# Optimization experiments

Hardware: AMD Instinct MI355X
Metric: run time of the kernel (lower is better)

Reference implementation:

```python
import jax, jax.numpy as jnp
import numpy as np

N_NODES = 100000
N_EDGES = 1600000
N_GRAPHS = 256
DIMS = [128, 128, 128, 128]  # gcn_layers_dim -> 3 GCNConv layers


def setup_inputs() -> dict:
    key = jax.random.key(0)
    ks = jax.random.split(key, 12)
    inp = {
        "x": jax.random.normal(ks[0], (N_NODES, DIMS[0]), jnp.float32),
        "edge_index": jax.random.randint(ks[1], (2, N_EDGES), 0, N_NODES),
        "edge_weight": jax.random.uniform(ks[2], (N_EDGES,), jnp.float32),
        "batch": jnp.sort(jax.random.randint(ks[3], (N_NODES,), 0, N_GRAPHS)),
    }
    for i in range(3):
        fan_in = DIMS[i]
        scale = 1.0 / np.sqrt(fan_in)
        inp[f"W{i+1}"] = jax.random.uniform(ks[4 + 2 * i], (DIMS[i], DIMS[i + 1]),
                                             jnp.float32, -scale, scale)
        inp[f"b{i+1}"] = jax.random.uniform(ks[5 + 2 * i], (DIMS[i + 1],),
                                             jnp.float32, -scale, scale)
    return inp


def reference(x, edge_index, edge_weight, batch, W1, b1, W2, b2, W3, b3):
    n = x.shape[0]
    # PyG GCNConv: add self-loops with weight 1, symmetric normalization.
    loop = jnp.arange(n)
    row = jnp.concatenate([edge_index[0], loop])  # source nodes
    col = jnp.concatenate([edge_index[1], loop])  # target nodes (aggregation index)
    w = jnp.concatenate([edge_weight, jnp.ones((n,), x.dtype)])
    deg = jax.ops.segment_sum(w, col, num_segments=n)
    dinv = jnp.where(deg > 0, jax.lax.rsqrt(deg), jnp.zeros_like(deg))
    norm = dinv[row] * w * dinv[col]  # [E+N]

    # global_mean_pool setup
    counts = jax.ops.segment_sum(jnp.ones((n,), x.dtype), batch,
                                 num_segments=N_GRAPHS)
    counts = jnp.maximum(counts, 1.0)[:, None]

    def gcn_conv(h, W, b):
        hl = h @ W                      # linear projection first (PyG order)
        msg = hl[row] * norm[:, None]   # gather + edge scaling
        out = jax.ops.segment_sum(msg, col, num_segments=n)  # scatter-add
        return out + b

    embeddings = []
    h = x
    for W, b in ((W1, b1), (W2, b2), (W3, b3)):
        h = gcn_conv(h, W, b)
        h = jax.nn.relu(h)              # relu_layers_index = [0,1,2]
        emb = jax.ops.segment_sum(h, batch, num_segments=N_GRAPHS) / counts
        embeddings.append(emb)          # gep = global_mean_pool
    return tuple(embeddings)
```

## Files before the change

### kernel.cpp

```cpp
#include <hip/hip_runtime.h>


typedef short short8 __attribute__((ext_vector_type(8)));
typedef float f32x4  __attribute__((ext_vector_type(4)));

__device__ inline unsigned pack_bf16x2(float a, float b) {
    unsigned ua = __float_as_uint(a);
    ua = (ua + 0x7FFFu + ((ua >> 16) & 1u)) >> 16;
    unsigned ub = __float_as_uint(b);
    ub = (ub + 0x7FFFu + ((ub >> 16) & 1u)) >> 16;
    return ua | (ub << 16);
}
__device__ inline ushort bf16_1(float a) {
    unsigned ua = __float_as_uint(a);
    return (ushort)((ua + 0x7FFFu + ((ua >> 16) & 1u)) >> 16);
}
__device__ inline float bf_lo(unsigned u) { return __uint_as_float(u << 16); }
__device__ inline float bf_hi(unsigned u) { return __uint_as_float(u & 0xFFFF0000u); }


template <bool F32IN>
__device__ __forceinline__ void gemm_tile(const void* __restrict__ Hin,
                                          const ushort* __restrict__ WbT,
                                          unsigned* __restrict__ O, int M,
                                          int bid, unsigned* sOut) {
    int lane = threadIdx.x & 63;
    int wv = threadIdx.x >> 6;
    int quad = lane >> 4;
    int mrow = lane & 15;
    int m0 = bid * 128 + wv * 32;
    int r0 = m0 + mrow;
    int r1 = r0 + 16;
    int r0c = r0 < M ? r0 : M - 1;
    int r1c = r1 < M ? r1 : M - 1;

    short8 a0[4], a1[4];
    if (F32IN) {
        const float* Hf = (const float*)Hin;
#pragma unroll
        for (int s = 0; s < 4; s++) {
            const float4* p0 = (const float4*)(Hf + (size_t)r0c * 128 + s * 32 + quad * 8);
            const float4* p1 = (const float4*)(Hf + (size_t)r1c * 128 + s * 32 + quad * 8);
            float4 f0 = p0[0], f1 = p0[1];
            float4 g0 = p1[0], g1 = p1[1];
            union { short8 s8; unsigned u[4]; } t0, t1;
            t0.u[0] = pack_bf16x2(f0.x, f0.y); t0.u[1] = pack_bf16x2(f0.z, f0.w);
            t0.u[2] = pack_bf16x2(f1.x, f1.y); t0.u[3] = pack_bf16x2(f1.z, f1.w);
            t1.u[0] = pack_bf16x2(g0.x, g0.y); t1.u[1] = pack_bf16x2(g0.z, g0.w);
            t1.u[2] = pack_bf16x2(g1.x, g1.y); t1.u[3] = pack_bf16x2(g1.z, g1.w);
            a0[s] = t0.s8; a1[s] = t1.s8;
        }
    } else {
        const unsigned* Hb = (const unsigned*)Hin;
#pragma unroll
        for (int s = 0; s < 4; s++) {
            a0[s] = *(const short8*)(Hb + (size_t)r0c * 64 + s * 16 + quad * 4);
            a1[s] = *(const short8*)(Hb + (size_t)r1c * 64 + s * 16 + quad * 4);
        }
    }
    f32x4 acc0[8], acc1[8];
#pragma unroll
    for (int t = 0; t < 8; t++) {
        acc0[t] = (f32x4){0.f, 0.f, 0.f, 0.f};
        acc1[t] = (f32x4){0.f, 0.f, 0.f, 0.f};
    }
#pragma unroll
    for (int s = 0; s < 4; s++) {
#pragma unroll
        for (int t = 0; t < 8; t++) {
            short8 b = *(const short8*)(WbT + (t * 16 + mrow) * 128 + s * 32 + quad * 8);
            acc0[t] = __builtin_amdgcn_mfma_f32_16x16x32_bf16(a0[s], b, acc0[t], 0, 0, 0);
            acc1[t] = __builtin_amdgcn_mfma_f32_16x16x32_bf16(a1[s], b, acc1[t], 0, 0, 0);
        }
    }
    ushort* so = (ushort*)(sOut + wv * 32 * 64);
#pragma unroll
    for (int t = 0; t < 8; t++) {
#pragma unroll
        for (int r = 0; r < 4; r++) {
            int lr = quad * 4 + r;
            int c = t * 16 + mrow;
            so[lr * 128 + c] = bf16_1(acc0[t][r]);
            so[(lr + 16) * 128 + c] = bf16_1(acc1[t][r]);
        }
    }
    __syncthreads();
    const unsigned* si = sOut + wv * 32 * 64;
#pragma unroll 8
    for (int r = 0; r < 32; r++) {
        int row = m0 + r;
        if (row < M) O[(size_t)row * 64 + lane] = si[r * 64 + lane];
    }
}

__device__ __forceinline__ void pool_tile(const unsigned* __restrict__ HB,
                                          const int* __restrict__ gb,
                                          float* __restrict__ outp, int g,
                                          float* part) {
    int lane = threadIdx.x & 63, w = threadIdx.x >> 6;
    int s = gb[g], e = gb[g + 1];
    float ax = 0.f, ay = 0.f;
    for (int i = s + w; i < e; i += 4) {
        unsigned u = HB[(size_t)i * 64 + lane];
        ax += bf_lo(u); ay += bf_hi(u);
    }
    part[w * 128 + lane * 2] = ax;
    part[w * 128 + lane * 2 + 1] = ay;
    __syncthreads();
    if (threadIdx.x < 128) {
        float sum = part[threadIdx.x] + part[128 + threadIdx.x]
                  + part[256 + threadIdx.x] + part[384 + threadIdx.x];
        float c = (float)(e - s);
        outp[g * 128 + threadIdx.x] = sum / fmaxf(c, 1.0f);
    }
}


__global__ void k_prep(const int* __restrict__ batch, int* __restrict__ gb,
                       int G, int N,
                       const float* __restrict__ W0, const float* __restrict__ W1,
                       const float* __restrict__ W2, ushort* __restrict__ WbT) {
    int id = blockIdx.x * blockDim.x + threadIdx.x;
    if (id <= G) {
        int lo = 0, hi = N;
        while (lo < hi) { int mid = (lo + hi) >> 1; if (batch[mid] < id) lo = mid + 1; else hi = mid; }
        gb[id] = lo;
    }
    if (id < 3 * 16384) {
        int l = id >> 14;
        const float* W = (l == 0) ? W0 : ((l == 1) ? W1 : W2);
        int id2 = id & 16383;
        int n = id2 & 127, k = id2 >> 7;
        WbT[l * 16384 + n * 128 + k] = bf16_1(W[k * 128 + n]);
    }
}

__global__ __launch_bounds__(256) void k_phase1(const int* __restrict__ ei,
                                                int* __restrict__ hist, int E,
                                                const float* __restrict__ x,
                                                const ushort* __restrict__ WbT,
                                                unsigned* __restrict__ O, int M,
                                                int nbGemm, int nbCount) {
    __shared__ unsigned sBuf[8192];
    if (blockIdx.x < nbGemm) {
        gemm_tile<true>(x, WbT, O, M, blockIdx.x, sBuf);
        return;
    }
    int blk = blockIdx.x - nbGemm;
    unsigned* hcnt = sBuf;
    int t = threadIdx.x;
    for (int i = t; i < nbGemm; i += 256) hcnt[i] = 0;
    __syncthreads();
    int base = blk * 8192;
    for (int i = t; i < 8192; i += 256) {
        int e = base + i;
        if (e < E) atomicAdd(&hcnt[(unsigned)ei[E + e] >> 7], 1u);
    }
    __syncthreads();
    for (int b = t; b < nbGemm; b += 256)
        hist[b * nbCount + blk] = (int)hcnt[b];
}

__global__ __launch_bounds__(1024) void k_scan1(const int* __restrict__ cnt,
                                                int* __restrict__ pre,
                                                int* __restrict__ bsum, int n) {
    __shared__ int wsum[16];
    int t = threadIdx.x, lane = t & 63, w = t >> 6;
    int i = blockIdx.x * 1024 + t;
    int v = (i < n) ? cnt[i] : 0;
    int x = v;
#pragma unroll
    for (int off = 1; off < 64; off <<= 1) {
        int y = __shfl_up(x, off, 64);
        if (lane >= off) x += y;
    }
    if (lane == 63) wsum[w] = x;
    __syncthreads();
    int woff = 0, tot = 0;
#pragma unroll
    for (int q = 0; q < 16; q++) { int s = wsum[q]; if (q < w) woff += s; tot += s; }
    if (i < n) pre[i] = woff + x - v;
    if (t == 0) bsum[blockIdx.x] = tot;
}

__global__ __launch_bounds__(256) void k_scat(const int* __restrict__ ei,
                                              const float* __restrict__ ew,
                                              const int* __restrict__ pre,
                                              const int* __restrict__ bsumRaw,
                                              int* __restrict__ bucketStart,
                                              int2* __restrict__ recs,
                                              int E, int nbkt, int nbCount,
                                              int nbScan) {
    __shared__ int sRaw[256];
    __shared__ int sPre[256];
    __shared__ int sWt[4];
    __shared__ int sBase[784];
    __shared__ unsigned rk[784];
    int t = threadIdx.x;
    sRaw[t] = (t < nbScan) ? bsumRaw[t] : 0;
    for (int b = t; b < nbkt; b += 256) rk[b] = 0;
    __syncthreads();
    int lane = t & 63, w2 = t >> 6;
    int v = sRaw[t];
    int x = v;
#pragma unroll
    for (int off = 1; off < 64; off <<= 1) {
        int y = __shfl_up(x, off, 64);
        if (lane >= off) x += y;
    }
    if (lane == 63) sWt[w2] = x;
    __syncthreads();
    int base = 0;
#pragma unroll
    for (int q = 0; q < 4; q++) { if (q < w2) base += sWt[q]; }
    sPre[t] = base + x - v;
    __syncthreads();
    int blk = blockIdx.x;
    for (int b = t; b < nbkt; b += 256) {
        int f = b * nbCount + blk;
        sBase[b] = pre[f] + sPre[f >> 10];
    }
    if (blk == 0) {
        for (int b = t; b <= nbkt; b += 256) {
            if (b == nbkt) bucketStart[b] = E;
            else { int f = b * nbCount; bucketStart[b] = pre[f] + sPre[f >> 10]; }
        }
    }
    __syncthreads();
    int e0 = blk * 8192;
    for (int i = t; i < 8192; i += 256) {
        int e = e0 + i;
        if (e < E) {
            int r = ei[e];
            int c = ei[E + e];
            float w = ew[e];
            int b = (unsigned)c >> 7;
            unsigned rank = atomicAdd(&rk[b], 1u);
            int2 rec; rec.x = r | ((c & 127) << 17); rec.y = __float_as_int(w);
            recs[sBase[b] + (int)rank] = rec;
        }
    }
}

__global__ __launch_bounds__(256) void k_fin(const int2* __restrict__ recs,
                                             const int* __restrict__ bucketStart,
                                             int2* __restrict__ csr,
                                             int* __restrict__ ptrv,
                                             float* __restrict__ dinv,
                                             int N, int nbkt) {
    __shared__ unsigned scnt[128];
    __shared__ float swdeg[128];
    __shared__ float sdinv[128];
    __shared__ unsigned sTot0;
    int t = threadIdx.x;
    int b = blockIdx.x;
    int e0 = bucketStart[b], e1 = bucketStart[b + 1];
    int FB = e0 + b * 128;
    if (t < 128) { scnt[t] = 0u; swdeg[t] = 0.f; }
    __syncthreads();
    for (int i = e0 + t; i < e1; i += 256) {
        int2 rec = recs[i];
        int cl = (rec.x >> 17) & 127;
        atomicAdd(&scnt[cl], 1u);
        atomicAdd(&swdeg[cl], __int_as_float(rec.y));
    }
    __syncthreads();
    unsigned myc = (t < 128) ? scnt[t] : 0u;
    int lane = t & 63, wv = t >> 6;
    unsigned inc = myc;
#pragma unroll
    for (int off = 1; off < 64; off <<= 1) {
        unsigned y = __shfl_up(inc, off, 64);
        if (lane >= off) inc += y;
    }
    if (t == 63) sTot0 = inc;
    __syncthreads();
    unsigned excl = inc - myc + ((wv == 1) ? sTot0 : 0u);
    if (t < 128) {
        float dv = rsqrtf(1.0f + swdeg[t]);
        sdinv[t] = dv;
        scnt[t] = excl + (unsigned)t + 1u;
        int node = b * 128 + t;
        int start = FB + (int)excl + t;
        if (node < N) {
            ptrv[node] = start;
            dinv[node] = dv;
            int2 sv; sv.x = node << 4;
            sv.y = __float_as_int(dv);
            csr[start] = sv;
        }
    }
    if (b == nbkt - 1 && t == 0) ptrv[N] = e1 + N;
    __syncthreads();
    for (int i = e0 + t; i < e1; i += 256) {
        int2 rec = recs[i];
        int cl = (rec.x >> 17) & 127;
        int r = rec.x & 131071;
        unsigned rank = atomicAdd(&scnt[cl], 1u);
        float y = __int_as_float(rec.y) * sdinv[cl];
        int2 mv; mv.x = r << 4; mv.y = __float_as_int(y);
        csr[FB + (int)rank] = mv;
    }
}

template <bool NORM>
__global__ __launch_bounds__(256) void k_agg(const unsigned* __restrict__ HL,
                                             const int* __restrict__ ptr,
                                             int2* __restrict__ csr,
                                             const float* __restrict__ dinv,
                                             const float* __restrict__ bias,
                                             unsigned* __restrict__ Hout, int M) {
    __shared__ int2 sM[4 * 64];
    int node = (int)((blockIdx.x * blockDim.x + threadIdx.x) >> 6);
    if (node >= M) return;
    int lane = threadIdx.x & 63;
    int grp = lane >> 4;
    int q = lane & 15;
    int2* mbase = &sM[(threadIdx.x >> 6) * 64];
    int e0 = ptr[node], e1 = ptr[node + 1];
    int deg = e1 - e0;
    int nbv = deg < 64 ? deg : 64;
    if (lane < nbv) {
        int2 m = csr[e0 + lane];
        if (NORM) {
            m.y = __float_as_int(__int_as_float(m.y) * dinv[m.x >> 4]);
            csr[e0 + lane] = m;
        }
        mbase[lane] = m;
    }
    const uint4* HL4 = (const uint4*)HL;
    float a0 = 0.f, a1 = 0.f, a2 = 0.f, a3 = 0.f;
    float a4 = 0.f, a5 = 0.f, a6 = 0.f, a7 = 0.f;
    int j = grp;
    for (; j + 16 <= nbv; j += 16) {
        int2 m[4]; uint4 u[4];
#pragma unroll
        for (int t = 0; t < 4; t++) m[t] = mbase[j + 4 * t];
#pragma unroll
        for (int t = 0; t < 4; t++) u[t] = HL4[(unsigned)(m[t].x + q)];
#pragma unroll
        for (int t = 0; t < 4; t++) {
            float nv = __int_as_float(m[t].y);
            a0 += nv * bf_lo(u[t].x); a1 += nv * bf_hi(u[t].x);
            a2 += nv * bf_lo(u[t].y); a3 += nv * bf_hi(u[t].y);
            a4 += nv * bf_lo(u[t].z); a5 += nv * bf_hi(u[t].z);
            a6 += nv * bf_lo(u[t].w); a7 += nv * bf_hi(u[t].w);
        }
    }
    for (; j < nbv; j += 4) {
        int2 m = mbase[j];
        uint4 u = HL4[(unsigned)(m.x + q)];
        float nv = __int_as_float(m.y);
        a0 += nv * bf_lo(u.x); a1 += nv * bf_hi(u.x);
        a2 += nv * bf_lo(u.y); a3 += nv * bf_hi(u.y);
        a4 += nv * bf_lo(u.z); a5 += nv * bf_hi(u.z);
        a6 += nv * bf_lo(u.w); a7 += nv * bf_hi(u.w);
    }
    for (int e = e0 + 64 + grp; e < e1; e += 4) {
        int2 m = csr[e];
        if (NORM) {
            m.y = __float_as_int(__int_as_float(m.y) * dinv[m.x >> 4]);
            csr[e] = m;
        }
        uint4 u = HL4[(unsigned)(m.x + q)];
        float nv = __int_as_float(m.y);
        a0 += nv * bf_lo(u.x); a1 += nv * bf_hi(u.x);
        a2 += nv * bf_lo(u.y); a3 += nv * bf_hi(u.y);
        a4 += nv * bf_lo(u.z); a5 += nv * bf_hi(u.z);
        a6 += nv * bf_lo(u.w); a7 += nv * bf_hi(u.w);
    }
    a0 += __shfl_xor(a0, 32, 64); a1 += __shfl_xor(a1, 32, 64);
    a2 += __shfl_xor(a2, 32, 64); a3 += __shfl_xor(a3, 32, 64);
    a4 += __shfl_xor(a4, 32, 64); a5 += __shfl_xor(a5, 32, 64);
    a6 += __shfl_xor(a6, 32, 64); a7 += __shfl_xor(a7, 32, 64);
    a0 += __shfl_xor(a0, 16, 64); a1 += __shfl_xor(a1, 16, 64);
    a2 += __shfl_xor(a2, 16, 64); a3 += __shfl_xor(a3, 16, 64);
    a4 += __shfl_xor(a4, 16, 64); a5 += __shfl_xor(a5, 16, 64);
    a6 += __shfl_xor(a6, 16, 64); a7 += __shfl_xor(a7, 16, 64);
    if (grp == 0) {
        const float4* b4 = (const float4*)bias;
        float4 bA = b4[2 * q], bB = b4[2 * q + 1];
        float r0 = fmaxf(a0 + bA.x, 0.f);
        float r1 = fmaxf(a1 + bA.y, 0.f);
        float r2 = fmaxf(a2 + bA.z, 0.f);
        float r3 = fmaxf(a3 + bA.w, 0.f);
        float r4 = fmaxf(a4 + bB.x, 0.f);
        float r5 = fmaxf(a5 + bB.y, 0.f);
        float r6 = fmaxf(a6 + bB.z, 0.f);
        float r7 = fmaxf(a7 + bB.w, 0.f);
        uint4 pv;
        pv.x = pack_bf16x2(r0, r1);
        pv.y = pack_bf16x2(r2, r3);
        pv.z = pack_bf16x2(r4, r5);
        pv.w = pack_bf16x2(r6, r7);
        ((uint4*)(Hout + (size_t)node * 64))[q] = pv;
    }
}

__global__ __launch_bounds__(256) void k_gemm_pool(const unsigned* __restrict__ Hb,
                                                   const ushort* __restrict__ WbT,
                                                   unsigned* __restrict__ O, int M,
                                                   const int* __restrict__ gb,
                                                   float* __restrict__ outp,
                                                   int nbGemm) {
    __shared__ unsigned sBuf[8192];
    if (blockIdx.x < nbGemm) {
        gemm_tile<false>(Hb, WbT, O, M, blockIdx.x, sBuf);
        return;
    }
    pool_tile(Hb, gb, outp, blockIdx.x - nbGemm, (float*)sBuf);
}

extern "C" void kernel_launch(void* const* d_in, const int* in_sizes, int n_in,
                              void* d_out, int out_size, void* d_ws, size_t ws_size,
                              hipStream_t stream) {
    const float* x     = (const float*)d_in[0];
    const int*   ei    = (const int*)d_in[1];
    const float* ew    = (const float*)d_in[2];
    const int*   batch = (const int*)d_in[3];
    const float* Wt[3] = {(const float*)d_in[4], (const float*)d_in[6], (const float*)d_in[8]};
    const float* bt[3] = {(const float*)d_in[5], (const float*)d_in[7], (const float*)d_in[9]};
    float* out = (float*)d_out;

    const int D = 128;
    const int N = in_sizes[0] / D;
    const int E = in_sizes[2];
    const int G = out_size / (3 * D);

    char* p = (char*)d_ws;
    auto alloc = [&](size_t bytes) {
        void* r = (void*)p;
        p += (bytes + 255) & ~(size_t)255;
        return r;
    };
    int nbkt    = (N + 127) / 128;
    int nbCount = (E + 8191) / 8192;
    int F       = nbkt * nbCount;
    int nbScan  = (F + 1023) / 1024;

    int*      ptr    = (int*)alloc((size_t)(N + 1) * 4);
    int*      bsum   = (int*)alloc((size_t)256 * 4);
    int*      gb     = (int*)alloc((size_t)(G + 1) * 4);
    int*      bstart = (int*)alloc((size_t)(nbkt + 1) * 4);
    float*    dinv   = (float*)alloc((size_t)N * 4);
    ushort*   WbT    = (ushort*)alloc((size_t)3 * 16384 * 2);
    int2*     csr    = (int2*)alloc((size_t)(E + N) * 8);
    unsigned* bufA   = (unsigned*)alloc((size_t)N * 64 * 4);
    unsigned* bufB   = (unsigned*)alloc((size_t)N * 64 * 4);
    int*  hist = (int*)csr;
    int*  pre  = hist + F;
    int2* recs = (int2*)bufB;

    int nbGemm = nbkt;
    int prepWork = 3 * 16384;

    k_prep<<<(prepWork + 255) / 256, 256, 0, stream>>>(batch, gb, G, N,
                                                       Wt[0], Wt[1], Wt[2], WbT);
    k_phase1<<<nbGemm + nbCount, 256, 0, stream>>>(ei, hist, E, x, WbT,
                                                   bufA, N, nbGemm, nbCount);
    k_scan1<<<nbScan, 1024, 0, stream>>>(hist, pre, bsum, F);
    k_scat<<<nbCount, 256, 0, stream>>>(ei, ew, pre, bsum, bstart, recs,
                                        E, nbkt, nbCount, nbScan);
    k_fin<<<nbkt, 256, 0, stream>>>(recs, bstart, csr, ptr, dinv, N, nbkt);

    k_agg<true><<<(N + 3) / 4, 256, 0, stream>>>(bufA, ptr, csr, dinv, bt[0],
                                                 bufB, N);
    k_gemm_pool<<<nbGemm + G, 256, 0, stream>>>(bufB, WbT + 16384, bufA, N,
                                                gb, out + 0 * (size_t)G * D, nbGemm);
    k_agg<false><<<(N + 3) / 4, 256, 0, stream>>>(bufA, ptr, csr, dinv, bt[1],
                                                  bufB, N);
    k_gemm_pool<<<nbGemm + G, 256, 0, stream>>>(bufB, WbT + 2 * 16384, bufA, N,
                                                gb, out + 1 * (size_t)G * D, nbGemm);
    k_agg<false><<<(N + 3) / 4, 256, 0, stream>>>(bufA, ptr, csr, dinv, bt[2],
                                                  bufB, N);
    k_gemm_pool<<<G, 256, 0, stream>>>(bufB, WbT, nullptr, 0,
                                       gb, out + 2 * (size_t)G * D, 0);
}
```

Baseline: 509.6 us.

## Split aggregation feature dimension across two block halves, recompute normalization

The aggregation kernel now launches twice as many blocks. Each half handles 64 of the 128 bf16 features, with 8 lanes per feature slice and 8 edge groups per wavefront instead of 16 lanes and 4 groups. The first-layer write-back of normalized weights into the CSR is removed, and every layer recomputes dinv[src] per edge, so the CSR becomes read-only. This raises parallelism and edge-level concurrency per node. In exchange, CSR and dinv reads are duplicated across halves, an extra shuffle reduction stage is added, and the halves read feature rows less contiguously.

```diff
diff --git a/kernel.cpp b/kernel.cpp
--- a/kernel.cpp
+++ b/kernel.cpp
@@ -303,29 +303,29 @@
     }
 }
 
-template <bool NORM>
 __global__ __launch_bounds__(256) void k_agg(const unsigned* __restrict__ HL,
                                              const int* __restrict__ ptr,
-                                             int2* __restrict__ csr,
+                                             const int2* __restrict__ csr,
                                              const float* __restrict__ dinv,
                                              const float* __restrict__ bias,
-                                             unsigned* __restrict__ Hout, int M) {
+                                             unsigned* __restrict__ Hout, int M,
+                                             int nbHalf) {
     __shared__ int2 sM[4 * 64];
-    int node = (int)((blockIdx.x * blockDim.x + threadIdx.x) >> 6);
+    int half = blockIdx.x >= nbHalf ? 1 : 0;
+    int bid = blockIdx.x - half * nbHalf;
+    int node = (int)(((size_t)bid * blockDim.x + threadIdx.x) >> 6);
     if (node >= M) return;
     int lane = threadIdx.x & 63;
-    int grp = lane >> 4;
-    int q = lane & 15;
+    int grp = lane >> 3;
+    int q = lane & 7;
+    int hb = half * 8 + q;
     int2* mbase = &sM[(threadIdx.x >> 6) * 64];
     int e0 = ptr[node], e1 = ptr[node + 1];
     int deg = e1 - e0;
     int nbv = deg < 64 ? deg : 64;
     if (lane < nbv) {
         int2 m = csr[e0 + lane];
-        if (NORM) {
-            m.y = __float_as_int(__int_as_float(m.y) * dinv[m.x >> 4]);
-            csr[e0 + lane] = m;
-        }
+        m.y = __float_as_int(__int_as_float(m.y) * dinv[m.x >> 4]);
         mbase[lane] = m;
     }
     const uint4* HL4 = (const uint4*)HL;
@@ -333,36 +333,33 @@
     float a4 = 0.f, a5 = 0.f, a6 = 0.f, a7 = 0.f;
     int j = grp;
     for (; j + 16 <= nbv; j += 16) {
-        int2 m[4]; uint4 u[4];
-#pragma unroll
-        for (int t = 0; t < 4; t++) m[t] = mbase[j + 4 * t];
-#pragma unroll
-        for (int t = 0; t < 4; t++) u[t] = HL4[(unsigned)(m[t].x + q)];
-#pragma unroll
-        for (int t = 0; t < 4; t++) {
-            float nv = __int_as_float(m[t].y);
-            a0 += nv * bf_lo(u[t].x); a1 += nv * bf_hi(u[t].x);
-            a2 += nv * bf_lo(u[t].y); a3 += nv * bf_hi(u[t].y);
-            a4 += nv * bf_lo(u[t].z); a5 += nv * bf_hi(u[t].z);
-            a6 += nv * bf_lo(u[t].w); a7 += nv * bf_hi(u[t].w);
-        }
-    }
-    for (; j < nbv; j += 4) {
+        int2 m0 = mbase[j], m1 = mbase[j + 8];
+        uint4 u0 = HL4[(unsigned)(m0.x + hb)];
+        uint4 u1 = HL4[(unsigned)(m1.x + hb)];
+        float n0 = __int_as_float(m0.y);
+        float n1 = __int_as_float(m1.y);
+        a0 += n0 * bf_lo(u0.x); a1 += n0 * bf_hi(u0.x);
+        a2 += n0 * bf_lo(u0.y); a3 += n0 * bf_hi(u0.y);
+        a4 += n0 * bf_lo(u0.z); a5 += n0 * bf_hi(u0.z);
+        a6 += n0 * bf_lo(u0.w); a7 += n0 * bf_hi(u0.w);
+        a0 += n1 * bf_lo(u1.x); a1 += n1 * bf_hi(u1.x);
+        a2 += n1 * bf_lo(u1.y); a3 += n1 * bf_hi(u1.y);
+        a4 += n1 * bf_lo(u1.z); a5 += n1 * bf_hi(u1.z);
+        a6 += n1 * bf_lo(u1.w); a7 += n1 * bf_hi(u1.w);
+    }
+    for (; j < nbv; j += 8) {
         int2 m = mbase[j];
-        uint4 u = HL4[(unsigned)(m.x + q)];
+        uint4 u = HL4[(unsigned)(m.x + hb)];
         float nv = __int_as_float(m.y);
         a0 += nv * bf_lo(u.x); a1 += nv * bf_hi(u.x);
         a2 += nv * bf_lo(u.y); a3 += nv * bf_hi(u.y);
         a4 += nv * bf_lo(u.z); a5 += nv * bf_hi(u.z);
         a6 += nv * bf_lo(u.w); a7 += nv * bf_hi(u.w);
     }
-    for (int e = e0 + 64 + grp; e < e1; e += 4) {
+    for (int e = e0 + 64 + grp; e < e1; e += 8) {
         int2 m = csr[e];
-        if (NORM) {
-            m.y = __float_as_int(__int_as_float(m.y) * dinv[m.x >> 4]);
-            csr[e] = m;
-        }
-        uint4 u = HL4[(unsigned)(m.x + q)];
+        m.y = __float_as_int(__int_as_float(m.y) * dinv[m.x >> 4]);
+        uint4 u = HL4[(unsigned)(m.x + hb)];
         float nv = __int_as_float(m.y);
         a0 += nv * bf_lo(u.x); a1 += nv * bf_hi(u.x);
         a2 += nv * bf_lo(u.y); a3 += nv * bf_hi(u.y);
@@ -377,9 +374,13 @@
     a2 += __shfl_xor(a2, 16, 64); a3 += __shfl_xor(a3, 16, 64);
     a4 += __shfl_xor(a4, 16, 64); a5 += __shfl_xor(a5, 16, 64);
     a6 += __shfl_xor(a6, 16, 64); a7 += __shfl_xor(a7, 16, 64);
+    a0 += __shfl_xor(a0, 8, 64);  a1 += __shfl_xor(a1, 8, 64);
+    a2 += __shfl_xor(a2, 8, 64);  a3 += __shfl_xor(a3, 8, 64);
+    a4 += __shfl_xor(a4, 8, 64);  a5 += __shfl_xor(a5, 8, 64);
+    a6 += __shfl_xor(a6, 8, 64);  a7 += __shfl_xor(a7, 8, 64);
     if (grp == 0) {
         const float4* b4 = (const float4*)bias;
-        float4 bA = b4[2 * q], bB = b4[2 * q + 1];
+        float4 bA = b4[2 * hb], bB = b4[2 * hb + 1];
         float r0 = fmaxf(a0 + bA.x, 0.f);
         float r1 = fmaxf(a1 + bA.y, 0.f);
         float r2 = fmaxf(a2 + bA.z, 0.f);
@@ -393,7 +394,7 @@
         pv.y = pack_bf16x2(r2, r3);
         pv.z = pack_bf16x2(r4, r5);
         pv.w = pack_bf16x2(r6, r7);
-        ((uint4*)(Hout + (size_t)node * 64))[q] = pv;
+        ((uint4*)(Hout + (size_t)node * 64))[hb] = pv;
     }
 }
 
@@ -452,6 +453,7 @@
     int2* recs = (int2*)bufB;
 
     int nbGemm = nbkt;
+    int nbHalf = (N + 3) / 4;
     int prepWork = 3 * 16384;
 
     k_prep<<<(prepWork + 255) / 256, 256, 0, stream>>>(batch, gb, G, N,
@@ -463,16 +465,16 @@
                                         E, nbkt, nbCount, nbScan);
     k_fin<<<nbkt, 256, 0, stream>>>(recs, bstart, csr, ptr, dinv, N, nbkt);
 
-    k_agg<true><<<(N + 3) / 4, 256, 0, stream>>>(bufA, ptr, csr, dinv, bt[0],
-                                                 bufB, N);
+    k_agg<<<2 * nbHalf, 256, 0, stream>>>(bufA, ptr, csr, dinv, bt[0],
+                                          bufB, N, nbHalf);
     k_gemm_pool<<<nbGemm + G, 256, 0, stream>>>(bufB, WbT + 16384, bufA, N,
                                                 gb, out + 0 * (size_t)G * D, nbGemm);
-    k_agg<false><<<(N + 3) / 4, 256, 0, stream>>>(bufA, ptr, csr, dinv, bt[1],
-                                                  bufB, N);
+    k_agg<<<2 * nbHalf, 256, 0, stream>>>(bufA, ptr, csr, dinv, bt[1],
+                                          bufB, N, nbHalf);
     k_gemm_pool<<<nbGemm + G, 256, 0, stream>>>(bufB, WbT + 2 * 16384, bufA, N,
                                                 gb, out + 1 * (size_t)G * D, nbGemm);
-    k_agg<false><<<(N + 3) / 4, 256, 0, stream>>>(bufA, ptr, csr, dinv, bt[2],
-                                                  bufB, N);
+    k_agg<<<2 * nbHalf, 256, 0, stream>>>(bufA, ptr, csr, dinv, bt[2],
+                                          bufB, N, nbHalf);
     k_gemm_pool<<<G, 256, 0, stream>>>(bufB, WbT, nullptr, 0,
                                        gb, out + 2 * (size_t)G * D, 0);
 }
```

Result: slower. 593.5 us (+16.5%).

## Merge prep into histogram kernel and co-schedule first GEMM with scatter

Applied to the files above, without the earlier changes.

The weight conversion and graph-boundary search now run as extra blocks inside the edge-histogram kernel, removing one launch. The first-layer GEMM moves out of the histogram kernel and runs in the same grid as the edge scatter, which uses shared memory carved from the GEMM buffer. This saves a kernel launch and changes which work overlaps. The larger shared allocation in the histogram kernel may lower its occupancy, and the scatter blocks now carry the GEMM's 32KB shared footprint.

```diff
diff --git a/kernel.cpp b/kernel.cpp
--- a/kernel.cpp
+++ b/kernel.cpp
@@ -116,40 +116,35 @@
 }
 
 
-__global__ void k_prep(const int* __restrict__ batch, int* __restrict__ gb,
-                       int G, int N,
-                       const float* __restrict__ W0, const float* __restrict__ W1,
-                       const float* __restrict__ W2, ushort* __restrict__ WbT) {
-    int id = blockIdx.x * blockDim.x + threadIdx.x;
-    if (id <= G) {
-        int lo = 0, hi = N;
-        while (lo < hi) { int mid = (lo + hi) >> 1; if (batch[mid] < id) lo = mid + 1; else hi = mid; }
-        gb[id] = lo;
-    }
-    if (id < 3 * 16384) {
-        int l = id >> 14;
-        const float* W = (l == 0) ? W0 : ((l == 1) ? W1 : W2);
-        int id2 = id & 16383;
-        int n = id2 & 127, k = id2 >> 7;
-        WbT[l * 16384 + n * 128 + k] = bf16_1(W[k * 128 + n]);
-    }
-}
-
-__global__ __launch_bounds__(256) void k_phase1(const int* __restrict__ ei,
-                                                int* __restrict__ hist, int E,
-                                                const float* __restrict__ x,
-                                                const ushort* __restrict__ WbT,
-                                                unsigned* __restrict__ O, int M,
-                                                int nbGemm, int nbCount) {
-    __shared__ unsigned sBuf[8192];
-    if (blockIdx.x < nbGemm) {
-        gemm_tile<true>(x, WbT, O, M, blockIdx.x, sBuf);
+__global__ __launch_bounds__(256) void k_hist_prep(const int* __restrict__ ei,
+                                                   int* __restrict__ hist, int E,
+                                                   int nbkt, int nbCount,
+                                                   const int* __restrict__ batch,
+                                                   int* __restrict__ gb, int G, int N,
+                                                   const float* __restrict__ W0,
+                                                   const float* __restrict__ W1,
+                                                   const float* __restrict__ W2,
+                                                   ushort* __restrict__ WbT) {
+    __shared__ unsigned hcnt[8192];
+    int t = threadIdx.x;
+    if (blockIdx.x >= nbCount) {
+        int id = (blockIdx.x - nbCount) * 256 + t;
+        if (id <= G) {
+            int lo = 0, hi = N;
+            while (lo < hi) { int mid = (lo + hi) >> 1; if (batch[mid] < id) lo = mid + 1; else hi = mid; }
+            gb[id] = lo;
+        }
+        if (id < 3 * 16384) {
+            int l = id >> 14;
+            const float* W = (l == 0) ? W0 : ((l == 1) ? W1 : W2);
+            int id2 = id & 16383;
+            int n = id2 & 127, k = id2 >> 7;
+            WbT[l * 16384 + n * 128 + k] = bf16_1(W[k * 128 + n]);
+        }
         return;
     }
-    int blk = blockIdx.x - nbGemm;
-    unsigned* hcnt = sBuf;
-    int t = threadIdx.x;
-    for (int i = t; i < nbGemm; i += 256) hcnt[i] = 0;
+    int blk = blockIdx.x;
+    for (int i = t; i < nbkt; i += 256) hcnt[i] = 0;
     __syncthreads();
     int base = blk * 8192;
     for (int i = t; i < 8192; i += 256) {
@@ -157,7 +152,7 @@
         if (e < E) atomicAdd(&hcnt[(unsigned)ei[E + e] >> 7], 1u);
     }
     __syncthreads();
-    for (int b = t; b < nbGemm; b += 256)
+    for (int b = t; b < nbkt; b += 256)
         hist[b * nbCount + blk] = (int)hcnt[b];
 }
 
@@ -183,39 +178,48 @@
     if (t == 0) bsum[blockIdx.x] = tot;
 }
 
-__global__ __launch_bounds__(256) void k_scat(const int* __restrict__ ei,
-                                              const float* __restrict__ ew,
-                                              const int* __restrict__ pre,
-                                              const int* __restrict__ bsumRaw,
-                                              int* __restrict__ bucketStart,
-                                              int2* __restrict__ recs,
-                                              int E, int nbkt, int nbCount,
-                                              int nbScan) {
-    __shared__ int sRaw[256];
-    __shared__ int sPre[256];
-    __shared__ int sWt[4];
-    __shared__ int sBase[784];
-    __shared__ unsigned rk[784];
+__global__ __launch_bounds__(256) void k_scat_gemm(const int* __restrict__ ei,
+                                                   const float* __restrict__ ew,
+                                                   const int* __restrict__ pre,
+                                                   const int* __restrict__ bsumRaw,
+                                                   int* __restrict__ bucketStart,
+                                                   int2* __restrict__ recs,
+                                                   int E, int nbkt, int nbCount,
+                                                   int nbScan,
+                                                   const float* __restrict__ x,
+                                                   const ushort* __restrict__ WbT,
+                                                   unsigned* __restrict__ O, int M,
+                                                   int nbGemm) {
+    __shared__ unsigned sBuf[8192];
+    if (blockIdx.x < nbGemm) {
+        gemm_tile<true>(x, WbT, O, M, blockIdx.x, sBuf);
+        return;
+    }
+    int* sRaw = (int*)sBuf;
+    int* sPre = sRaw + 256;
+    int* sWt  = sPre + 256;
+    int* sBase = sWt + 4;
+    unsigned* rk = (unsigned*)(sBase + 784);
     int t = threadIdx.x;
     sRaw[t] = (t < nbScan) ? bsumRaw[t] : 0;
     for (int b = t; b < nbkt; b += 256) rk[b] = 0;
     __syncthreads();
     int lane = t & 63, w2 = t >> 6;
     int v = sRaw[t];
-    int x = v;
+    int xv = v;
 #pragma unroll
     for (int off = 1; off < 64; off <<= 1) {
-        int y = __shfl_up(x, off, 64);
-        if (lane >= off) x += y;
-    }
-    if (lane == 63) sWt[w2] = x;
+        int y = __shfl_up(xv, off, 64);
+        if (lane >= off) xv += y;
+    }
+    if (lane == 63) sWt[w2] = xv;
     __syncthreads();
     int base = 0;
 #pragma unroll
     for (int q = 0; q < 4; q++) { if (q < w2) base += sWt[q]; }
-    sPre[t] = base + x - v;
-    __syncthreads();
-    int blk = blockIdx.x;
+    sPre[t] = base + xv - v;
+    __syncthreads();
+    int blk = blockIdx.x - nbGemm;
     for (int b = t; b < nbkt; b += 256) {
         int f = b * nbCount + blk;
         sBase[b] = pre[f] + sPre[f >> 10];
@@ -452,15 +456,16 @@
     int2* recs = (int2*)bufB;
 
     int nbGemm = nbkt;
-    int prepWork = 3 * 16384;
-
-    k_prep<<<(prepWork + 255) / 256, 256, 0, stream>>>(batch, gb, G, N,
-                                                       Wt[0], Wt[1], Wt[2], WbT);
-    k_phase1<<<nbGemm + nbCount, 256, 0, stream>>>(ei, hist, E, x, WbT,
-                                                   bufA, N, nbGemm, nbCount);
+    int nbPrep = (3 * 16384 + 255) / 256;
+
+    k_hist_prep<<<nbCount + nbPrep, 256, 0, stream>>>(ei, hist, E, nbkt, nbCount,
+                                                      batch, gb, G, N,
+                                                      Wt[0], Wt[1], Wt[2], WbT);
     k_scan1<<<nbScan, 1024, 0, stream>>>(hist, pre, bsum, F);
-    k_scat<<<nbCount, 256, 0, stream>>>(ei, ew, pre, bsum, bstart, recs,
-                                        E, nbkt, nbCount, nbScan);
+    k_scat_gemm<<<nbGemm + nbCount, 256, 0, stream>>>(ei, ew, pre, bsum, bstart,
+                                                      recs, E, nbkt, nbCount,
+                                                      nbScan, x, WbT, bufA, N,
+                                                      nbGemm);
     k_fin<<<nbkt, 256, 0, stream>>>(recs, bstart, csr, ptr, dinv, N, nbkt);
 
     k_agg<true><<<(N + 3) / 4, 256, 0, stream>>>(bufA, ptr, csr, dinv, bt[0],
```

After: 498.6 us. 1.02x faster.
